# Kernel tuning notes

Measured on AMD Instinct MI355X. Metric: run time of the kernel, lower is better.

Reference implementation:

```python
import jax, jax.numpy as jnp
import numpy as np

BINWIDTHS = (5000, 1000, 500, 200, 100, 50, 25)
WINDOW = (0, 200000)
TOTAL = WINDOW[1] - WINDOW[0]

def _level_shapes():
    shapes = []
    cw = TOTAL
    for bw in BINWIDTHS:
        nb = cw // bw
        ns = TOTAL // (bw * nb)
        shapes.append((ns, nb))
        cw = bw
    return shapes

LEVEL_SHAPES = _level_shapes()          # [(1,40),(40,5),(200,2),(500,2),(1000,2),(2000,2),(4000,2)]
NBINS = [ns * nb for ns, nb in LEVEL_SHAPES]
N_FINAL = TOTAL // BINWIDTHS[-1]        # 8000

N_REGIONS = 500
N_CLUSTERS = 20
N_REGIONS_OI = 256
N_CELLS = 10000
N_CUTS = 500000
DELTA_P_SCALE = 1.5


def setup_inputs() -> dict:
    key = jax.random.key(0)
    ks = jax.random.split(key, 32)
    inp = {}
    inp["components"] = jax.random.normal(ks[0], (N_CLUSTERS, N_CLUSTERS), jnp.float32)
    for lvl, (ns, nb) in enumerate(LEVEL_SHAPES):
        inp[f"w_bias_{lvl}"] = jax.random.normal(ks[1 + lvl], (N_REGIONS, ns, nb), jnp.float32) * 0.05
        inp[f"w_delta_{lvl}"] = jax.random.normal(ks[10 + lvl], (N_REGIONS, N_CLUSTERS, ns * nb), jnp.float32) * 0.02
    inp["regions_oi"] = jax.random.randint(ks[20], (N_REGIONS_OI,), 0, N_REGIONS)
    inp["local_region_ix"] = jax.random.randint(ks[21], (N_CUTS,), 0, N_REGIONS_OI)
    inp["local_cell_ix"] = jax.random.randint(ks[22], (N_CUTS,), 0, N_CELLS)
    inp["clustering_indices"] = jax.random.randint(ks[23], (N_CELLS,), 0, N_CLUSTERS)
    inp["coordinates"] = jax.random.randint(ks[24], (N_CUTS,), WINDOW[0], WINDOW[1])
    return inp


def _calculate_w(components, w_biases, w_deltas, regions_oi):
    R = regions_oi.shape[0]
    C = components.shape[1]
    scale = jnp.float32(DELTA_P_SCALE)
    log_scale = jnp.log(scale)
    half_log_2pi = jnp.float32(0.5 * np.log(2.0 * np.pi))
    w = jnp.zeros((R, C, N_FINAL), jnp.float32)
    kl = jnp.float32(0.0)
    for lvl, (ns, nb) in enumerate(LEVEL_SHAPES):
        wb = w_biases[lvl][regions_oi]                    # (R, ns, nb) irregular gather
        Wd = w_deltas[lvl][regions_oi]                    # (R, C, ns*nb) irregular gather
        # MultiLinear: einsum('ab,cad->cbd', components, W)
        wd = jnp.einsum('ab,cad->cbd', components, Wd)    # (R, C, ns*nb)
        wd = wd.reshape(R, C, ns, nb)
        w_level = (wb[:, None, :, :] + wd).reshape(R, C, NBINS[lvl])
        rep = N_FINAL // NBINS[lvl]
        w = (w.reshape(R, C, NBINS[lvl], rep) + w_level[..., None]).reshape(R, C, N_FINAL)
        # Normal(0, scale).log_prob(wd), summed
        kl = kl + jnp.sum(-0.5 * (wd / scale) ** 2 - log_scale - half_log_2pi)
    w = jax.nn.log_softmax(w, axis=-1) - jnp.log(jnp.float32(BINWIDTHS[-1]))
    return w, kl


def reference(components, w_bias_0, w_bias_1, w_bias_2, w_bias_3, w_bias_4, w_bias_5, w_bias_6,
              w_delta_0, w_delta_1, w_delta_2, w_delta_3, w_delta_4, w_delta_5, w_delta_6,
              regions_oi, local_region_ix, local_cell_ix, clustering_indices, coordinates):
    w_biases = [w_bias_0, w_bias_1, w_bias_2, w_bias_3, w_bias_4, w_bias_5, w_bias_6]
    w_deltas = [w_delta_0, w_delta_1, w_delta_2, w_delta_3, w_delta_4, w_delta_5, w_delta_6]
    w, kl = _calculate_w(components, w_biases, w_deltas, regions_oi)
    coords = jnp.clip(coordinates, WINDOW[0], WINDOW[1] - 1) - WINDOW[0]
    bin_ix = coords // BINWIDTHS[-1]
    cluster_ix = clustering_indices[local_cell_ix]
    likelihood = w[local_region_ix, cluster_ix, bin_ix]   # (N_CUTS,)
    return likelihood, kl
```

## Files before the change

kernel.cpp:

```cpp
#include <hip/hip_runtime.h>
#include <hip/hip_bf16.h>
#include <math.h>


#define NROI 256
#define NC 20
#define NFINAL 8000
#define NCUTS 500000
#define TB 256
#define NTILE 32
#define UTSTR 40
#define NKL (NROI * NTILE + NROI)

typedef __attribute__((ext_vector_type(8))) short bf16x8;
typedef __attribute__((ext_vector_type(4))) float f32x4;

static __device__ __forceinline__ ushort bfr(float x) {
    union { __hip_bfloat16 h; ushort u; } v;
    v.h = __float2bfloat16(x);
    return v.u;
}
static __device__ __forceinline__ bf16x8 pack8(float4 a, float4 b) {
    union { bf16x8 v; ushort s[8]; } u;
    u.s[0] = bfr(a.x); u.s[1] = bfr(a.y); u.s[2] = bfr(a.z); u.s[3] = bfr(a.w);
    u.s[4] = bfr(b.x); u.s[5] = bfr(b.y); u.s[6] = bfr(b.z); u.s[7] = bfr(b.w);
    return u.v;
}

__global__ void k_init(const float* __restrict__ comp,
                       float* __restrict__ g2, float* __restrict__ gfull,
                       ushort* __restrict__ compPad)
{
    const int tid = threadIdx.x;
    for (int i = tid; i < 400; i += 256) {
        const int a = i / 20, b = i % 20;
        float s = 0.f;
#pragma unroll
        for (int c = 0; c < 20; c++) s += comp[a * 20 + c] * comp[b * 20 + c];
        g2[i] = (b < a) ? 0.f : (b == a ? s : 2.f * s);
    }
    for (int i = tid; i < 1024; i += 256) {
        const int rr = i >> 5, cc = i & 31;
        float s = 0.f;
        if (rr < 20 && cc < 20) {
#pragma unroll
            for (int c = 0; c < 20; c++) s += comp[rr * 20 + c] * comp[cc * 20 + c];
        }
        gfull[i] = s;
        const float v = (rr < 20 && cc < 20) ? comp[cc * 20 + rr] : 0.f;
        compPad[i] = bfr(v);
    }
}

__global__ __launch_bounds__(256, 2) void k_main(
    const float* __restrict__ gfull, const ushort* __restrict__ compPad,
    const float* __restrict__ wb0, const float* __restrict__ wd0,
    const float* __restrict__ wb1, const float* __restrict__ wd1,
    const float* __restrict__ wb2, const float* __restrict__ wd2,
    const float* __restrict__ wb3, const float* __restrict__ wd3,
    const float* __restrict__ wb4, const float* __restrict__ wd4,
    const float* __restrict__ wb5, const float* __restrict__ wd5,
    const float* __restrict__ wb6, const float* __restrict__ wd6,
    const int* __restrict__ regions_oi,
    __hip_bfloat16* __restrict__ w2,
    float* __restrict__ s_part, float* __restrict__ klbuf)
{
    __shared__ ushort Utsh[TB * UTSTR];
    __shared__ float cs_sh[20 * 64];
    __shared__ float biasf[TB];
    __shared__ float sexp_sh[20];
    __shared__ float klp[4];

    const int tid = threadIdx.x;
    const int wv = tid >> 6, ln = tid & 63;
    const int l15 = ln & 15, lg = ln >> 4;
    const int r = blockIdx.x >> 5;
    const int tile = blockIdx.x & 31;
    const int base = tile << 8;
    const int r0 = regions_oi[r];

    const float* __restrict__ p6 = wd6 + (size_t)r0 * (20 * 8000);
    const float* __restrict__ p5 = wd5 + (size_t)r0 * (20 * 4000);
    const float* __restrict__ p4 = wd4 + (size_t)r0 * (20 * 2000);
    const float* __restrict__ p3 = wd3 + (size_t)r0 * (20 * 1000);
    const float* __restrict__ p2 = wd2 + (size_t)r0 * (20 * 400);
    const float* __restrict__ p1 = wd1 + (size_t)r0 * (20 * 200);
    const float* __restrict__ p0 = wd0 + (size_t)r0 * (20 * 40);
    const float* __restrict__ b6 = wb6 + (size_t)r0 * 8000;
    const float* __restrict__ b5 = wb5 + (size_t)r0 * 4000;
    const float* __restrict__ b4 = wb4 + (size_t)r0 * 2000;
    const float* __restrict__ b3 = wb3 + (size_t)r0 * 1000;
    const float* __restrict__ b2 = wb2 + (size_t)r0 * 400;
    const float* __restrict__ b1 = wb1 + (size_t)r0 * 200;
    const float* __restrict__ b0 = wb0 + (size_t)r0 * 40;

    if (tid < 20) sexp_sh[tid] = 0.f;

#pragma unroll 1
    for (int it = 0; it < 5; it++) {
        const int u = it * 256 + tid;
        const int a = u >> 6, qd = u & 63;
        const int j = base + 4 * qd;
        float v = 0.f;
        if (j < NFINAL)
            v = p4[a * 2000 + (j >> 2)] + p3[a * 1000 + (j >> 3)]
              + p2[a * 400 + j / 20] + p1[a * 200 + j / 40]
              + p0[a * 40 + j / 200];
        cs_sh[a * 64 + qd] = v;
    }
    {
        const int j = base + tid;
        float v = 0.f;
        if (j < NFINAL)
            v = b6[j] + b5[j >> 1] + b4[j >> 2] + b3[j >> 3]
              + b2[j / 20] + b1[j / 40] + b0[j / 200];
        biasf[tid] = v;
    }
    __syncthreads();

    {
        const int j = base + tid;
        const bool ok = j < NFINAL;
        const int qd = tid >> 2;
#pragma unroll 1
        for (int it = 0; it < 5; it++) {
            float u[4];
#pragma unroll
            for (int i = 0; i < 4; i++) {
                const int a = 4 * it + i;
                float x6 = 0.f, x5 = 0.f;
                if (ok) {
                    x6 = p6[(size_t)a * 8000 + j];
                    x5 = p5[a * 4000 + (j >> 1)];
                }
                u[i] = x6 + x5 + cs_sh[a * 64 + qd];
            }
            *(ushort4*)&Utsh[tid * UTSTR + 4 * it] =
                make_ushort4(bfr(u[0]), bfr(u[1]), bfr(u[2]), bfr(u[3]));
        }
        const ushort4 z4 = make_ushort4(0, 0, 0, 0);
        *(ushort4*)&Utsh[tid * UTSTR + 20] = z4;
        *(ushort4*)&Utsh[tid * UTSTR + 24] = z4;
        *(ushort4*)&Utsh[tid * UTSTR + 28] = z4;
    }
    __syncthreads();

    {
        f32x4 s00 = {0.f, 0.f, 0.f, 0.f};
        f32x4 s10 = {0.f, 0.f, 0.f, 0.f};
        f32x4 s11 = {0.f, 0.f, 0.f, 0.f};
#pragma unroll 1
        for (int ch = wv; ch < 15; ch += 4) {
            const float* P; int K, col0;
            if (ch < 8)       { P = p6; K = 8000; col0 = base + ch * 32; }
            else if (ch < 12) { P = p5; K = 4000; col0 = (base >> 1) + (ch - 8) * 32; }
            else if (ch < 14) { P = p4; K = 2000; col0 = (base >> 2) + (ch - 12) * 32; }
            else              { P = p3; K = 1000; col0 = (base >> 3); }
            const int cb = col0 + lg * 8;
            bf16x8 flo = {0,0,0,0,0,0,0,0}, fhi = {0,0,0,0,0,0,0,0};
            if (cb < K) {
                const float4 xa = *(const float4*)(P + (size_t)l15 * K + cb);
                const float4 xb = *(const float4*)(P + (size_t)l15 * K + cb + 4);
                flo = pack8(xa, xb);
                if (l15 < 4) {
                    const float4 ya = *(const float4*)(P + (size_t)(16 + l15) * K + cb);
                    const float4 yb = *(const float4*)(P + (size_t)(16 + l15) * K + cb + 4);
                    fhi = pack8(ya, yb);
                }
            }
            s00 = __builtin_amdgcn_mfma_f32_16x16x32_bf16(flo, flo, s00, 0, 0, 0);
            s10 = __builtin_amdgcn_mfma_f32_16x16x32_bf16(fhi, flo, s10, 0, 0, 0);
            s11 = __builtin_amdgcn_mfma_f32_16x16x32_bf16(fhi, fhi, s11, 0, 0, 0);
        }
        float qp = 0.f;
#pragma unroll
        for (int reg = 0; reg < 4; reg++) {
            const int rlo = lg * 4 + reg, rhi = 16 + lg * 4 + reg;
            qp += gfull[rlo * 32 + l15] * s00[reg];
            qp += 2.f * gfull[rhi * 32 + l15] * s10[reg];
            qp += gfull[rhi * 32 + 16 + l15] * s11[reg];
        }
#pragma unroll
        for (int off = 32; off > 0; off >>= 1) qp += __shfl_down(qp, off, 64);
        if (ln == 0) klp[wv] = qp;
    }

    {
        bf16x8 fA0 = *(const bf16x8*)&compPad[l15 * 32 + lg * 8];
        bf16x8 fA1 = *(const bf16x8*)&compPad[(16 + l15) * 32 + lg * 8];
        float sA[4] = {0.f, 0.f, 0.f, 0.f};
        float sB[4] = {0.f, 0.f, 0.f, 0.f};
#pragma unroll 1
        for (int t = 0; t < 4; t++) {
            const int nt = 4 * t + wv;
            bf16x8 fB = *(const bf16x8*)&Utsh[(nt * 16 + l15) * UTSTR + lg * 8];
            const f32x4 z = {0.f, 0.f, 0.f, 0.f};
            f32x4 c0 = __builtin_amdgcn_mfma_f32_16x16x32_bf16(fA0, fB, z, 0, 0, 0);
            f32x4 c1 = __builtin_amdgcn_mfma_f32_16x16x32_bf16(fA1, fB, z, 0, 0, 0);
            const int binl = nt * 16 + l15;
            const int bin = base + binl;
            const float bi = biasf[binl];
            if (bin < NFINAL) {
#pragma unroll
                for (int reg = 0; reg < 4; reg++) {
                    const int c = lg * 4 + reg;
                    const float w = bi + c0[reg];
                    w2[(size_t)(r * 20 + c) * 8000 + bin] = __float2bfloat16(w);
                    sA[reg] += __expf(w);
                }
                if (lg == 0) {
#pragma unroll
                    for (int reg = 0; reg < 4; reg++) {
                        const float w = bi + c1[reg];
                        w2[(size_t)(r * 20 + 16 + reg) * 8000 + bin] = __float2bfloat16(w);
                        sB[reg] += __expf(w);
                    }
                }
            }
        }
#pragma unroll
        for (int reg = 0; reg < 4; reg++) {
            float s = sA[reg];
            s += __shfl_xor(s, 1, 64); s += __shfl_xor(s, 2, 64);
            s += __shfl_xor(s, 4, 64); s += __shfl_xor(s, 8, 64);
            if (l15 == 0) atomicAdd(&sexp_sh[lg * 4 + reg], s);
            float sb = sB[reg];
            sb += __shfl_xor(sb, 1, 64); sb += __shfl_xor(sb, 2, 64);
            sb += __shfl_xor(sb, 4, 64); sb += __shfl_xor(sb, 8, 64);
            if (ln == 0) atomicAdd(&sexp_sh[16 + reg], sb);
        }
    }
    __syncthreads();
    if (tid < 20) s_part[((size_t)r * NTILE + tile) * 20 + tid] = sexp_sh[tid];
    if (tid == 0) klbuf[blockIdx.x] = klp[0] + klp[1] + klp[2] + klp[3];
}

__global__ __launch_bounds__(256, 2) void k_klc(
    const float* __restrict__ g2,
    const float* __restrict__ wd0, const float* __restrict__ wd1,
    const float* __restrict__ wd2,
    const int* __restrict__ regions_oi, float* __restrict__ klbuf)
{
    __shared__ float klp[4];
    const int tid = threadIdx.x;
    const int r0 = regions_oi[blockIdx.x];
    const float* __restrict__ p2 = wd2 + (size_t)r0 * (20 * 400);
    const float* __restrict__ p1 = wd1 + (size_t)r0 * (20 * 200);
    const float* __restrict__ p0 = wd0 + (size_t)r0 * (20 * 40);

    float q = 0.f;
#pragma unroll 1
    for (int it = 0; it < 3; it++) {
        const int u = it * 256 + tid;
        if (u >= 640) break;
        const float* P; int K, col;
        if (u < 400)      { P = p2; K = 400; col = u; }
        else if (u < 600) { P = p1; K = 200; col = u - 400; }
        else              { P = p0; K = 40;  col = u - 600; }
        float x[20];
#pragma unroll
        for (int a = 0; a < 20; a++) x[a] = P[a * K + col];
#pragma unroll
        for (int a = 0; a < 20; a++) {
            float t = g2[a * 21] * x[a];
#pragma unroll
            for (int b = a + 1; b < 20; b++) t += g2[a * 20 + b] * x[b];
            q += x[a] * t;
        }
    }
#pragma unroll
    for (int off = 32; off > 0; off >>= 1) q += __shfl_down(q, off, 64);
    if ((tid & 63) == 0) klp[tid >> 6] = q;
    __syncthreads();
    if (tid == 0)
        klbuf[NROI * NTILE + blockIdx.x] = klp[0] + klp[1] + klp[2] + klp[3];
}

__global__ void k_klred(const float* __restrict__ klbuf, float* __restrict__ kl)
{
    __shared__ float part[4];
    const int tid = threadIdx.x;
    float s = 0.f;
    for (int i = tid; i < NKL; i += 256) s += klbuf[i];
#pragma unroll
    for (int off = 32; off > 0; off >>= 1) s += __shfl_down(s, off, 64);
    if ((tid & 63) == 0) part[tid >> 6] = s;
    __syncthreads();
    if (tid == 0)
        kl[0] = (float)(-80076800.0 * 1.3244036413128371)
              + (part[0] + part[1] + part[2] + part[3]) * (-0.5f / 2.25f);
}

__global__ void k_sub(const float* __restrict__ s_part, float* __restrict__ sub)
{
    const int i = blockIdx.x * 256 + threadIdx.x;
    if (i >= NROI * NC) return;
    const int r = i / 20, c = i % 20;
    float s = 0.f;
#pragma unroll 1
    for (int t = 0; t < NTILE; t++) s += s_part[(size_t)(r * NTILE + t) * 20 + c];
    sub[i] = logf(s) + 3.2188758248682006f;
}

__global__ void k_gather(const int* __restrict__ lri, const int* __restrict__ lci,
                         const int* __restrict__ cli, const int* __restrict__ coords,
                         const __hip_bfloat16* __restrict__ w2,
                         const float* __restrict__ sub,
                         float* __restrict__ out)
{
    const int i = blockIdx.x * 256 + threadIdx.x;
    if (i >= NCUTS) return;
    const int r = lri[i];
    const int c = cli[lci[i]];
    int co = coords[i];
    co = co < 0 ? 0 : (co > 199999 ? 199999 : co);
    const int bin = co / 25;
    const int rc = r * 20 + c;
    out[i] = __bfloat162float(w2[(size_t)rc * 8000 + bin]) - sub[rc];
}

extern "C" void kernel_launch(void* const* d_in, const int* in_sizes, int n_in,
                              void* d_out, int out_size, void* d_ws, size_t ws_size,
                              hipStream_t stream)
{
    const float* comp = (const float*)d_in[0];
    const float* wb[7];
    const float* wd[7];
    if (in_sizes[2] == 400000) {
        for (int l = 0; l < 7; l++) { wb[l] = (const float*)d_in[1 + 2 * l]; wd[l] = (const float*)d_in[2 + 2 * l]; }
    } else {
        for (int l = 0; l < 7; l++) { wb[l] = (const float*)d_in[1 + l]; wd[l] = (const float*)d_in[8 + l]; }
    }
    const int* regions_oi = (const int*)d_in[15];
    const int* lri   = (const int*)d_in[16];
    const int* lci   = (const int*)d_in[17];
    const int* cli   = (const int*)d_in[18];
    const int* coords= (const int*)d_in[19];
    float* out = (float*)d_out;

    __hip_bfloat16* w2 = (__hip_bfloat16*)d_ws;
    float* s_part = (float*)(w2 + (size_t)NROI * NC * NFINAL);
    float* sub    = s_part + (size_t)NROI * NTILE * 20;
    float* g2buf  = sub + NROI * NC;
    float* gfull  = g2buf + 400;
    ushort* compPad = (ushort*)(gfull + 1024);
    float* klbuf  = (float*)(compPad + 1024);
    const size_t need = (size_t)NROI * NC * NFINAL * 2
                      + ((size_t)NROI * NTILE * 20 + NROI * NC + 400 + 1024 + 512
                         + NKL) * sizeof(float);
    if (ws_size < need) return;

    k_init<<<1, 256, 0, stream>>>(comp, g2buf, gfull, compPad);
    k_main<<<NROI * NTILE, 256, 0, stream>>>(gfull, compPad,
        wb[0], wd[0], wb[1], wd[1], wb[2], wd[2], wb[3], wd[3],
        wb[4], wd[4], wb[5], wd[5], wb[6], wd[6],
        regions_oi, w2, s_part, klbuf);
    k_klc<<<NROI, 256, 0, stream>>>(g2buf, wd[0], wd[1], wd[2],
        regions_oi, klbuf);
    k_klred<<<1, 256, 0, stream>>>(klbuf, out + NCUTS);
    k_sub<<<(NROI * NC + 255) / 256, 256, 0, stream>>>(s_part, sub);
    k_gather<<<(NCUTS + 255) / 256, 256, 0, stream>>>(lri, lci, cli, coords,
        w2, sub, out);
}
```

Measured before the change: 207.6 us.

## Stage all level slices in shared memory with vector loads and FP32 component matmul

Each block now loads every level's weight-delta and bias slice for its tile into one shared buffer with coalesced float4/float2 loads, instead of scattered per-element global reads with integer divisions. The per-level contributions are summed in place in shared memory. The bf16 MFMA projection through the components matrix is replaced by an FP32 FMA loop in which each wave computes five clusters over four bins per lane. That loop writes bf16 packs and per-cluster exp sums directly, with no shared atomics. This cuts global load instructions and bf16 rounding of the inputs, but adds scalar FMA work, more shared memory (about 42KB per block), and a larger register footprint.

```diff
diff --git a/kernel.cpp b/kernel.cpp
--- a/kernel.cpp
+++ b/kernel.cpp
@@ -9,8 +9,23 @@
 #define NCUTS 500000
 #define TB 256
 #define NTILE 32
-#define UTSTR 40
 #define NKL (NROI * NTILE + NROI)
+
+#define L6O 0
+#define L5O 5120
+#define L4O 7680
+#define L3O 8960
+#define L2O 9600
+#define L1O 9920
+#define L0O 10080
+#define B5O 10160
+#define B4O 10288
+#define B3O 10352
+#define B2O 10384
+#define B1O 10400
+#define B0O 10408
+#define BFO 10416
+#define SHSZ 10672
 
 typedef __attribute__((ext_vector_type(8))) short bf16x8;
 typedef __attribute__((ext_vector_type(4))) float f32x4;
@@ -29,7 +44,7 @@
 
 __global__ void k_init(const float* __restrict__ comp,
                        float* __restrict__ g2, float* __restrict__ gfull,
-                       ushort* __restrict__ compPad)
+                       float* __restrict__ compT)
 {
     const int tid = threadIdx.x;
     for (int i = tid; i < 400; i += 256) {
@@ -38,6 +53,7 @@
 #pragma unroll
         for (int c = 0; c < 20; c++) s += comp[a * 20 + c] * comp[b * 20 + c];
         g2[i] = (b < a) ? 0.f : (b == a ? s : 2.f * s);
+        compT[i] = comp[b * 20 + a];
     }
     for (int i = tid; i < 1024; i += 256) {
         const int rr = i >> 5, cc = i & 31;
@@ -47,13 +63,11 @@
             for (int c = 0; c < 20; c++) s += comp[rr * 20 + c] * comp[cc * 20 + c];
         }
         gfull[i] = s;
-        const float v = (rr < 20 && cc < 20) ? comp[cc * 20 + rr] : 0.f;
-        compPad[i] = bfr(v);
     }
 }
 
 __global__ __launch_bounds__(256, 2) void k_main(
-    const float* __restrict__ gfull, const ushort* __restrict__ compPad,
+    const float* __restrict__ gfull, const float* __restrict__ compT,
     const float* __restrict__ wb0, const float* __restrict__ wd0,
     const float* __restrict__ wb1, const float* __restrict__ wd1,
     const float* __restrict__ wb2, const float* __restrict__ wd2,
@@ -65,10 +79,7 @@
     __hip_bfloat16* __restrict__ w2,
     float* __restrict__ s_part, float* __restrict__ klbuf)
 {
-    __shared__ ushort Utsh[TB * UTSTR];
-    __shared__ float cs_sh[20 * 64];
-    __shared__ float biasf[TB];
-    __shared__ float sexp_sh[20];
+    __shared__ float sh[SHSZ];
     __shared__ float klp[4];
 
     const int tid = threadIdx.x;
@@ -94,54 +105,143 @@
     const float* __restrict__ b1 = wb1 + (size_t)r0 * 200;
     const float* __restrict__ b0 = wb0 + (size_t)r0 * 40;
 
-    if (tid < 20) sexp_sh[tid] = 0.f;
-
-#pragma unroll 1
-    for (int it = 0; it < 5; it++) {
-        const int u = it * 256 + tid;
+    const int c2b = (base / 20) & ~3;
+    const int c1b = (base / 40) & ~1;
+    const int c0b = (base / 200) & ~1;
+
+#pragma unroll
+    for (int k = 0; k < 5; k++) {
+        const int u = tid + 256 * k;
+        const int a = u >> 6, q = u & 63;
+        const int j = base + 4 * q;
+        float4 v = make_float4(0.f, 0.f, 0.f, 0.f);
+        if (j < NFINAL) v = *(const float4*)(p6 + (size_t)a * 8000 + j);
+        *(float4*)&sh[L6O + a * 256 + 4 * q] = v;
+    }
+#pragma unroll
+    for (int k = 0; k < 3; k++) {
+        const int u = tid + 256 * k;
+        if (u < 640) {
+            const int a = u >> 5, q = u & 31;
+            const int col = (base >> 1) + 4 * q;
+            float4 v = make_float4(0.f, 0.f, 0.f, 0.f);
+            if (col < 4000) v = *(const float4*)(p5 + a * 4000 + col);
+            *(float4*)&sh[L5O + a * 128 + 4 * q] = v;
+        }
+    }
+#pragma unroll
+    for (int k = 0; k < 2; k++) {
+        const int u = tid + 256 * k;
+        if (u < 320) {
+            const int a = u >> 4, q = u & 15;
+            const int col = (base >> 2) + 4 * q;
+            float4 v = make_float4(0.f, 0.f, 0.f, 0.f);
+            if (col < 2000) v = *(const float4*)(p4 + a * 2000 + col);
+            *(float4*)&sh[L4O + a * 64 + 4 * q] = v;
+        }
+    }
+    if (tid < 160) {
+        const int a = tid >> 3, q = tid & 7;
+        const int col = (base >> 3) + 4 * q;
+        float4 v = make_float4(0.f, 0.f, 0.f, 0.f);
+        if (col < 1000) v = *(const float4*)(p3 + a * 1000 + col);
+        *(float4*)&sh[L3O + a * 32 + 4 * q] = v;
+    }
+    if (tid < 80) {
+        const int a = tid >> 2, q = tid & 3;
+        const int col = c2b + 4 * q;
+        float4 v = make_float4(0.f, 0.f, 0.f, 0.f);
+        if (col < 400) v = *(const float4*)(p2 + a * 400 + col);
+        *(float4*)&sh[L2O + a * 16 + 4 * q] = v;
+    }
+    if (tid < 80) {
+        const int a = tid >> 2, q = tid & 3;
+        const int col = c1b + 2 * q;
+        float2 v = make_float2(0.f, 0.f);
+        if (col < 200) v = *(const float2*)(p1 + a * 200 + col);
+        *(float2*)&sh[L1O + a * 8 + 2 * q] = v;
+    }
+    if (tid < 40) {
+        const int a = tid >> 1, q = tid & 1;
+        const int col = c0b + 2 * q;
+        float2 v = make_float2(0.f, 0.f);
+        if (col < 40) v = *(const float2*)(p0 + a * 40 + col);
+        *(float2*)&sh[L0O + a * 4 + 2 * q] = v;
+    }
+    if (tid < 64) {
+        const int j = base + 4 * tid;
+        float4 v = make_float4(0.f, 0.f, 0.f, 0.f);
+        if (j < NFINAL) v = *(const float4*)(b6 + j);
+        *(float4*)&sh[BFO + 4 * tid] = v;
+    }
+    if (tid < 32) {
+        const int col = (base >> 1) + 4 * tid;
+        float4 v = make_float4(0.f, 0.f, 0.f, 0.f);
+        if (col < 4000) v = *(const float4*)(b5 + col);
+        *(float4*)&sh[B5O + 4 * tid] = v;
+    }
+    if (tid < 16) {
+        const int col = (base >> 2) + 4 * tid;
+        float4 v = make_float4(0.f, 0.f, 0.f, 0.f);
+        if (col < 2000) v = *(const float4*)(b4 + col);
+        *(float4*)&sh[B4O + 4 * tid] = v;
+    }
+    if (tid < 8) {
+        const int col = (base >> 3) + 4 * tid;
+        float4 v = make_float4(0.f, 0.f, 0.f, 0.f);
+        if (col < 1000) v = *(const float4*)(b3 + col);
+        *(float4*)&sh[B3O + 4 * tid] = v;
+    }
+    if (tid < 4) {
+        const int col = c2b + 4 * tid;
+        float4 v = make_float4(0.f, 0.f, 0.f, 0.f);
+        if (col < 400) v = *(const float4*)(b2 + col);
+        *(float4*)&sh[B2O + 4 * tid] = v;
+    }
+    if (tid < 4) {
+        const int col = c1b + 2 * tid;
+        float2 v = make_float2(0.f, 0.f);
+        if (col < 200) v = *(const float2*)(b1 + col);
+        *(float2*)&sh[B1O + 2 * tid] = v;
+    }
+    if (tid < 2) {
+        const int col = c0b + 2 * tid;
+        float2 v = make_float2(0.f, 0.f);
+        if (col < 40) v = *(const float2*)(b0 + col);
+        *(float2*)&sh[B0O + 2 * tid] = v;
+    }
+    __syncthreads();
+
+#pragma unroll
+    for (int k = 0; k < 5; k++) {
+        const int u = tid + 256 * k;
         const int a = u >> 6, qd = u & 63;
         const int j = base + 4 * qd;
-        float v = 0.f;
-        if (j < NFINAL)
-            v = p4[a * 2000 + (j >> 2)] + p3[a * 1000 + (j >> 3)]
-              + p2[a * 400 + j / 20] + p1[a * 200 + j / 40]
-              + p0[a * 40 + j / 200];
-        cs_sh[a * 64 + qd] = v;
+        const float v = sh[L4O + a * 64 + qd] + sh[L3O + a * 32 + (qd >> 1)]
+                      + sh[L2O + a * 16 + (j / 20 - c2b)]
+                      + sh[L1O + a * 8 + (j / 40 - c1b)]
+                      + sh[L0O + a * 4 + (j / 200 - c0b)];
+        sh[L4O + a * 64 + qd] = v;
     }
     {
         const int j = base + tid;
-        float v = 0.f;
-        if (j < NFINAL)
-            v = b6[j] + b5[j >> 1] + b4[j >> 2] + b3[j >> 3]
-              + b2[j / 20] + b1[j / 40] + b0[j / 200];
-        biasf[tid] = v;
-    }
-    __syncthreads();
-
-    {
-        const int j = base + tid;
-        const bool ok = j < NFINAL;
-        const int qd = tid >> 2;
-#pragma unroll 1
-        for (int it = 0; it < 5; it++) {
-            float u[4];
-#pragma unroll
-            for (int i = 0; i < 4; i++) {
-                const int a = 4 * it + i;
-                float x6 = 0.f, x5 = 0.f;
-                if (ok) {
-                    x6 = p6[(size_t)a * 8000 + j];
-                    x5 = p5[a * 4000 + (j >> 1)];
-                }
-                u[i] = x6 + x5 + cs_sh[a * 64 + qd];
-            }
-            *(ushort4*)&Utsh[tid * UTSTR + 4 * it] =
-                make_ushort4(bfr(u[0]), bfr(u[1]), bfr(u[2]), bfr(u[3]));
-        }
-        const ushort4 z4 = make_ushort4(0, 0, 0, 0);
-        *(ushort4*)&Utsh[tid * UTSTR + 20] = z4;
-        *(ushort4*)&Utsh[tid * UTSTR + 24] = z4;
-        *(ushort4*)&Utsh[tid * UTSTR + 28] = z4;
+        const float add = sh[B5O + (tid >> 1)] + sh[B4O + (tid >> 2)]
+                        + sh[B3O + (tid >> 3)] + sh[B2O + (j / 20 - c2b)]
+                        + sh[B1O + (j / 40 - c1b)] + sh[B0O + (j / 200 - c0b)];
+        sh[BFO + tid] += add;
+    }
+    __syncthreads();
+
+#pragma unroll
+    for (int k = 0; k < 5; k++) {
+        const int u = tid + 256 * k;
+        const int a = u >> 6, q = u & 63;
+        float4 v6 = *(float4*)&sh[L6O + a * 256 + 4 * q];
+        const float2 v5 = *(const float2*)&sh[L5O + a * 128 + 2 * q];
+        const float cs = sh[L4O + a * 64 + q];
+        v6.x += v5.x + cs; v6.y += v5.x + cs;
+        v6.z += v5.y + cs; v6.w += v5.y + cs;
+        *(float4*)&sh[L6O + a * 256 + 4 * q] = v6;
     }
     __syncthreads();
 
@@ -186,52 +286,68 @@
     }
 
     {
-        bf16x8 fA0 = *(const bf16x8*)&compPad[l15 * 32 + lg * 8];
-        bf16x8 fA1 = *(const bf16x8*)&compPad[(16 + l15) * 32 + lg * 8];
-        float sA[4] = {0.f, 0.f, 0.f, 0.f};
-        float sB[4] = {0.f, 0.f, 0.f, 0.f};
-#pragma unroll 1
-        for (int t = 0; t < 4; t++) {
-            const int nt = 4 * t + wv;
-            bf16x8 fB = *(const bf16x8*)&Utsh[(nt * 16 + l15) * UTSTR + lg * 8];
-            const f32x4 z = {0.f, 0.f, 0.f, 0.f};
-            f32x4 c0 = __builtin_amdgcn_mfma_f32_16x16x32_bf16(fA0, fB, z, 0, 0, 0);
-            f32x4 c1 = __builtin_amdgcn_mfma_f32_16x16x32_bf16(fA1, fB, z, 0, 0, 0);
-            const int binl = nt * 16 + l15;
-            const int bin = base + binl;
-            const float bi = biasf[binl];
-            if (bin < NFINAL) {
-#pragma unroll
-                for (int reg = 0; reg < 4; reg++) {
-                    const int c = lg * 4 + reg;
-                    const float w = bi + c0[reg];
-                    w2[(size_t)(r * 20 + c) * 8000 + bin] = __float2bfloat16(w);
-                    sA[reg] += __expf(w);
+        const int cbase = __builtin_amdgcn_readfirstlane(wv * 5);
+        const float* __restrict__ cc = compT + cbase * 20;
+        const int j = base + 4 * ln;
+        const bool ok = j < NFINAL;
+        const float4 bi = *(const float4*)&sh[BFO + 4 * ln];
+        {
+            float4 a0 = bi, a1 = bi, a2 = bi;
+#pragma unroll
+            for (int a = 0; a < 20; a++) {
+                const float4 u = *(const float4*)&sh[L6O + a * 256 + 4 * ln];
+                const float f0 = cc[a], f1 = cc[20 + a], f2 = cc[40 + a];
+                a0.x += f0 * u.x; a0.y += f0 * u.y; a0.z += f0 * u.z; a0.w += f0 * u.w;
+                a1.x += f1 * u.x; a1.y += f1 * u.y; a1.z += f1 * u.z; a1.w += f1 * u.w;
+                a2.x += f2 * u.x; a2.y += f2 * u.y; a2.z += f2 * u.z; a2.w += f2 * u.w;
+            }
+            float4 accs[3] = {a0, a1, a2};
+#pragma unroll
+            for (int k = 0; k < 3; k++) {
+                float se = 0.f;
+                if (ok) {
+                    const float4 acc = accs[k];
+                    union { __hip_bfloat162 h2[2]; uint2 u2; } pk;
+                    pk.h2[0] = __float22bfloat162_rn(make_float2(acc.x, acc.y));
+                    pk.h2[1] = __float22bfloat162_rn(make_float2(acc.z, acc.w));
+                    *(uint2*)(w2 + (size_t)(r * 20 + cbase + k) * 8000 + j) = pk.u2;
+                    se = __expf(acc.x) + __expf(acc.y) + __expf(acc.z) + __expf(acc.w);
                 }
-                if (lg == 0) {
-#pragma unroll
-                    for (int reg = 0; reg < 4; reg++) {
-                        const float w = bi + c1[reg];
-                        w2[(size_t)(r * 20 + 16 + reg) * 8000 + bin] = __float2bfloat16(w);
-                        sB[reg] += __expf(w);
-                    }
+#pragma unroll
+                for (int off = 32; off > 0; off >>= 1) se += __shfl_down(se, off, 64);
+                if (ln == 0)
+                    s_part[((size_t)r * NTILE + tile) * 20 + cbase + k] = se;
+            }
+        }
+        {
+            float4 a0 = bi, a1 = bi;
+#pragma unroll
+            for (int a = 0; a < 20; a++) {
+                const float4 u = *(const float4*)&sh[L6O + a * 256 + 4 * ln];
+                const float f0 = cc[60 + a], f1 = cc[80 + a];
+                a0.x += f0 * u.x; a0.y += f0 * u.y; a0.z += f0 * u.z; a0.w += f0 * u.w;
+                a1.x += f1 * u.x; a1.y += f1 * u.y; a1.z += f1 * u.z; a1.w += f1 * u.w;
+            }
+            float4 accs[2] = {a0, a1};
+#pragma unroll
+            for (int k = 0; k < 2; k++) {
+                float se = 0.f;
+                if (ok) {
+                    const float4 acc = accs[k];
+                    union { __hip_bfloat162 h2[2]; uint2 u2; } pk;
+                    pk.h2[0] = __float22bfloat162_rn(make_float2(acc.x, acc.y));
+                    pk.h2[1] = __float22bfloat162_rn(make_float2(acc.z, acc.w));
+                    *(uint2*)(w2 + (size_t)(r * 20 + cbase + 3 + k) * 8000 + j) = pk.u2;
+                    se = __expf(acc.x) + __expf(acc.y) + __expf(acc.z) + __expf(acc.w);
                 }
+#pragma unroll
+                for (int off = 32; off > 0; off >>= 1) se += __shfl_down(se, off, 64);
+                if (ln == 0)
+                    s_part[((size_t)r * NTILE + tile) * 20 + cbase + 3 + k] = se;
             }
         }
-#pragma unroll
-        for (int reg = 0; reg < 4; reg++) {
-            float s = sA[reg];
-            s += __shfl_xor(s, 1, 64); s += __shfl_xor(s, 2, 64);
-            s += __shfl_xor(s, 4, 64); s += __shfl_xor(s, 8, 64);
-            if (l15 == 0) atomicAdd(&sexp_sh[lg * 4 + reg], s);
-            float sb = sB[reg];
-            sb += __shfl_xor(sb, 1, 64); sb += __shfl_xor(sb, 2, 64);
-            sb += __shfl_xor(sb, 4, 64); sb += __shfl_xor(sb, 8, 64);
-            if (ln == 0) atomicAdd(&sexp_sh[16 + reg], sb);
-        }
-    }
-    __syncthreads();
-    if (tid < 20) s_part[((size_t)r * NTILE + tile) * 20 + tid] = sexp_sh[tid];
+    }
+    __syncthreads();
     if (tid == 0) klbuf[blockIdx.x] = klp[0] + klp[1] + klp[2] + klp[3];
 }
 
@@ -343,15 +459,15 @@
     float* sub    = s_part + (size_t)NROI * NTILE * 20;
     float* g2buf  = sub + NROI * NC;
     float* gfull  = g2buf + 400;
-    ushort* compPad = (ushort*)(gfull + 1024);
-    float* klbuf  = (float*)(compPad + 1024);
+    float* compT  = gfull + 1024;
+    float* klbuf  = compT + 400;
     const size_t need = (size_t)NROI * NC * NFINAL * 2
-                      + ((size_t)NROI * NTILE * 20 + NROI * NC + 400 + 1024 + 512
+                      + ((size_t)NROI * NTILE * 20 + NROI * NC + 400 + 1024 + 400
                          + NKL) * sizeof(float);
     if (ws_size < need) return;
 
-    k_init<<<1, 256, 0, stream>>>(comp, g2buf, gfull, compPad);
-    k_main<<<NROI * NTILE, 256, 0, stream>>>(gfull, compPad,
+    k_init<<<1, 256, 0, stream>>>(comp, g2buf, gfull, compT);
+    k_main<<<NROI * NTILE, 256, 0, stream>>>(gfull, compT,
         wb[0], wd[0], wb[1], wd[1], wb[2], wd[2], wb[3], wd[3],
         wb[4], wd[4], wb[5], wd[5], wb[6], wd[6],
         regions_oi, w2, s_part, klbuf);
```

Result: slower. 259.9 us (+25.2%).
